# Performance work log

Measured on AMD Instinct MI355X. Metric: run time of the kernel, lower is better.

Reference implementation:

```python
import jax, jax.numpy as jnp
import numpy as np
from jax import lax

B, T = 32, 768
N_MEL = 80
ENC_POS = 544  # encoder_output_dim(512) + positional_embedding_dim(32)
PRE = 256
RNN = 1024


def setup_inputs() -> dict:
    key = jax.random.key(0)
    ks = jax.random.split(key, 12)
    n = lambda k, shape, s: jax.random.normal(k, shape, jnp.float32) * s
    return {
        'duration_outputs': n(ks[0], (B, T, ENC_POS), 1.0),
        'decoder_inputs': n(ks[1], (B, N_MEL, T), 1.0),
        'memory_lengths': jax.random.randint(ks[2], (B,), 1, T + 1, dtype=jnp.int32),
        'pre_w1': n(ks[3], (N_MEL, PRE), 0.05),
        'pre_w2': n(ks[4], (PRE, PRE), 0.05),
        'rnn1_wx': n(ks[5], (PRE + ENC_POS, 4 * RNN), 0.02),
        'rnn1_wh': n(ks[6], (RNN, 4 * RNN), 0.02),
        'rnn1_b': jnp.zeros(4 * RNN, jnp.float32),
        'rnn1_g': jnp.ones(4 * RNN, jnp.float32),
        'rnn1_bn': jnp.zeros(4 * RNN, jnp.float32),
        'rnn1_gc': jnp.ones(RNN, jnp.float32),
        'rnn1_bc': jnp.zeros(RNN, jnp.float32),
        'rnn2_wx': n(ks[7], (RNN, 4 * RNN), 0.02),
        'rnn2_wh': n(ks[8], (RNN, 4 * RNN), 0.02),
        'rnn2_b': jnp.zeros(4 * RNN, jnp.float32),
        'rnn2_g': jnp.ones(4 * RNN, jnp.float32),
        'rnn2_bn': jnp.zeros(4 * RNN, jnp.float32),
        'rnn2_gc': jnp.ones(RNN, jnp.float32),
        'rnn2_bc': jnp.zeros(RNN, jnp.float32),
        'proj_w': n(ks[9], (RNN + ENC_POS, N_MEL), 0.02),
        'proj_b': jnp.zeros(N_MEL, jnp.float32),
    }


def _ln(x, g, b):
    m = jnp.mean(x, axis=-1, keepdims=True)
    v = jnp.var(x, axis=-1, keepdims=True)
    return (x - m) * lax.rsqrt(v + 1e-5) * g + b


def _lstm_norm_cell(x, h, c, wx, wh, b, g, bn, gc, bc):
    # layer-normalized LSTM cell: LN over gate pre-activations + LN on cell
    z = _ln(x @ wx + h @ wh + b, g, bn)            # [B, 4H]
    i, f, gg, o = jnp.split(z, 4, axis=-1)
    c = jax.nn.sigmoid(f) * c + jax.nn.sigmoid(i) * jnp.tanh(gg)
    h = jax.nn.sigmoid(o) * jnp.tanh(_ln(c, gc, bc))
    return h, c


def reference(duration_outputs, decoder_inputs, memory_lengths,
              pre_w1, pre_w2,
              rnn1_wx, rnn1_wh, rnn1_b, rnn1_g, rnn1_bn, rnn1_gc, rnn1_bc,
              rnn2_wx, rnn2_wh, rnn2_b, rnn2_g, rnn2_bn, rnn2_gc, rnn2_bc,
              proj_w, proj_b):
    b = decoder_inputs.shape[0]
    t = decoder_inputs.shape[2]
    # parse_decoder_inputs: [B, M, T] -> [T, B, M]; prepend go frame
    dec = jnp.transpose(decoder_inputs, (2, 0, 1))
    dec = jnp.concatenate([jnp.zeros((1, b, N_MEL), dec.dtype), dec], axis=0)  # [T+1,B,M]
    # prenet (dropout disabled for deterministic reference)
    x = jax.nn.relu(dec @ pre_w1)
    x = jax.nn.relu(x @ pre_w2)
    pre = x[:t]                                            # [T, B, PRE]
    dur = jnp.transpose(duration_outputs, (1, 0, 2))       # [T, B, ENC_POS]

    def step(carry, xs):
        h1, c1, h2, c2 = carry
        p, d = xs
        cell_in = jnp.concatenate([p, d], axis=-1)
        h1, c1 = _lstm_norm_cell(cell_in, h1, c1, rnn1_wx, rnn1_wh, rnn1_b, rnn1_g, rnn1_bn, rnn1_gc, rnn1_bc)
        h2, c2 = _lstm_norm_cell(h1, h2, c2, rnn2_wx, rnn2_wh, rnn2_b, rnn2_g, rnn2_bn, rnn2_gc, rnn2_bc)
        out = jnp.concatenate([h2, d], axis=-1) @ proj_w + proj_b  # [B, M]
        return (h1, c1, h2, c2), out

    init = tuple(jnp.zeros((b, RNN), jnp.float32) for _ in range(4))
    _, mel = lax.scan(step, init, (pre, dur))              # [T, B, M]
    return jnp.transpose(mel, (1, 2, 0))                   # [B, M, T]
```

## Files before the change

### kernel.cpp

```cpp
#include <hip/hip_runtime.h>
#include <cstdint>
#include <cstddef>

typedef _Float16 f16;
typedef _Float16 f16x8 __attribute__((ext_vector_type(8)));
typedef float f32x4 __attribute__((ext_vector_type(4)));

#define MFMA_F16(a,b,c) __builtin_amdgcn_mfma_f32_16x16x32_f16((a),(b),(c),0,0,0)

#define LOG2E  1.4426950408889634f
#define LOG2E2 2.885390081777927f

__device__ __forceinline__ float sigf(float x){
  return __builtin_amdgcn_rcpf(1.f + exp2f(-x * LOG2E));
}
__device__ __forceinline__ float tanhfast(float x){
  float e = exp2f(x * LOG2E2);
  return fmaf(-2.f, __builtin_amdgcn_rcpf(e + 1.f), 1.f);
}

__device__ __forceinline__ void st_wt_f32(float* p, float v){
  asm volatile("global_store_dword %0, %1, off sc0 sc1" :: "v"(p), "v"(v) : "memory");
}
__device__ __forceinline__ void st_wt_u32(f16* p, unsigned v){
  asm volatile("global_store_dword %0, %1, off sc0 sc1" :: "v"(p), "v"(v) : "memory");
}
__device__ __forceinline__ void st_tag(unsigned* p, unsigned v){
  asm volatile("global_store_dword %0, %1, off sc0 sc1" :: "v"(p), "v"(v) : "memory");
}
__device__ __forceinline__ void tag_wait(const unsigned* p, unsigned target){
  for (;;){
    unsigned v;
    asm volatile("global_load_dword %0, %1, off sc0 sc1\n\ts_waitcnt vmcnt(0)"
                 : "=v"(v) : "v"(p) : "memory");
    if (v >= target) return;
    __builtin_amdgcn_s_sleep(1);
  }
}
__device__ __forceinline__ void vm_drain(){ asm volatile("s_waitcnt vmcnt(0)" ::: "memory"); }

template<int N> __device__ __forceinline__ void vm_waitN(){
  asm volatile("s_waitcnt vmcnt(%0)" :: "i"(N) : "memory");
  __builtin_amdgcn_sched_barrier(0);
}

__device__ __forceinline__ void ld_8f32(const float* p, f32x4& a, f32x4& b){
  asm volatile(
    "global_load_dwordx4 %0, %2, off sc0 sc1\n\t"
    "global_load_dwordx4 %1, %2, off offset:16 sc0 sc1\n\t"
    "s_waitcnt vmcnt(0)"
    : "=&v"(a), "=&v"(b) : "v"(p) : "memory");
}

__device__ __forceinline__ void ld8_issue(const f16* p, f16x8* f){
  asm volatile(
    "global_load_dwordx4 %0, %8, off sc0 sc1\n\t"
    "global_load_dwordx4 %1, %8, off offset:64 sc0 sc1\n\t"
    "global_load_dwordx4 %2, %8, off offset:128 sc0 sc1\n\t"
    "global_load_dwordx4 %3, %8, off offset:192 sc0 sc1\n\t"
    "global_load_dwordx4 %4, %8, off offset:256 sc0 sc1\n\t"
    "global_load_dwordx4 %5, %8, off offset:320 sc0 sc1\n\t"
    "global_load_dwordx4 %6, %8, off offset:384 sc0 sc1\n\t"
    "global_load_dwordx4 %7, %8, off offset:448 sc0 sc1"
    : "=&v"(f[0]),"=&v"(f[1]),"=&v"(f[2]),"=&v"(f[3]),
      "=&v"(f[4]),"=&v"(f[5]),"=&v"(f[6]),"=&v"(f[7])
    : "v"(p) : "memory");
}

__device__ __forceinline__ f32x4 gemm32r(const f16* hp, const f16x8* bfrag){
  f32x4 a = {0.f,0.f,0.f,0.f};
  f16x8 fA[8], fB[8];
  ld8_issue(hp,       fA);
  ld8_issue(hp + 256, fB);
  vm_waitN<8>();
  #pragma unroll
  for (int kk = 0; kk < 8; ++kk) a = MFMA_F16(fA[kk], bfrag[kk], a);
  ld8_issue(hp + 512, fA);
  vm_waitN<8>();
  #pragma unroll
  for (int kk = 0; kk < 8; ++kk) a = MFMA_F16(fB[kk], bfrag[8 + kk], a);
  ld8_issue(hp + 768, fB);
  vm_waitN<8>();
  #pragma unroll
  for (int kk = 0; kk < 8; ++kk) a = MFMA_F16(fA[kk], bfrag[16 + kk], a);
  vm_waitN<0>();
  #pragma unroll
  for (int kk = 0; kk < 8; ++kk) a = MFMA_F16(fB[kk], bfrag[24 + kk], a);
  return a;
}

__global__ __launch_bounds__(256) void k_transpose_f16(const float* __restrict__ src,
    f16* __restrict__ dst, int K, int N, int dstStride, int dstOff){
  const int n0 = blockIdx.x*32, k0 = blockIdx.y*32, tid = threadIdx.x;
  __shared__ float tl[32][33];
  #pragma unroll
  for (int rep = 0; rep < 4; ++rep){
    int e = rep*256 + tid; int i = e >> 5, j = e & 31;
    int k = k0 + i, n = n0 + j;
    tl[i][j] = (k < K && n < N) ? src[(size_t)k*N + n] : 0.f;
  }
  __syncthreads();
  #pragma unroll
  for (int rep = 0; rep < 4; ++rep){
    int e = rep*256 + tid; int i2 = e & 31, j2 = e >> 5;
    int n = n0 + j2, k = k0 + i2;
    if (k < K && n < N) dst[(size_t)n*dstStride + dstOff + k] = (f16)tl[i2][j2];
  }
}

__global__ __launch_bounds__(256) void k_prenet(const float* __restrict__ dec,
    const float* __restrict__ w1, const float* __restrict__ w2, f16* __restrict__ cellin){
  const int t = blockIdx.x, tid = threadIdx.x;
  __shared__ float sin_[32][81];
  __shared__ f16   w1T[256][88];
  __shared__ float x1s[32][260];
  __shared__ f16   w2c[256][72];
  __shared__ f16   xo[32][256];
  for (int e = tid; e < 32*80; e += 256){
    int i = e/80, m = e - i*80;
    sin_[i][m] = (t == 0) ? 0.f : dec[(size_t)i*61440 + (size_t)m*768 + (t-1)];
  }
  for (int e = tid; e < 80*256; e += 256){ int m = e >> 8, j = e & 255; w1T[j][m] = (f16)w1[e]; }
  __syncthreads();
  const int j = tid;
  for (int i = 0; i < 32; ++i){
    float a = 0.f;
    #pragma unroll
    for (int m8 = 0; m8 < 10; ++m8){
      f16x8 wvv = *(const f16x8*)&w1T[j][m8*8];
      #pragma unroll
      for (int l = 0; l < 8; ++l) a += (float)wvv[l] * sin_[i][m8*8 + l];
    }
    x1s[i][j] = fmaxf(a, 0.f);
  }
  __syncthreads();
  float acc2[32];
  #pragma unroll
  for (int i = 0; i < 32; ++i) acc2[i] = 0.f;
  for (int c = 0; c < 4; ++c){
    for (int e = tid; e < 64*256; e += 256){
      int kl = e >> 8, jj = e & 255;
      w2c[jj][kl] = (f16)w2[(size_t)(c*64 + kl)*256 + jj];
    }
    __syncthreads();
    f16x8 wv8[8];
    #pragma unroll
    for (int k8 = 0; k8 < 8; ++k8) wv8[k8] = *(const f16x8*)&w2c[j][k8*8];
    for (int i = 0; i < 32; ++i){
      float a = 0.f;
      #pragma unroll
      for (int k8 = 0; k8 < 8; ++k8)
        #pragma unroll
        for (int l = 0; l < 8; ++l) a += (float)wv8[k8][l]*x1s[i][c*64 + k8*8 + l];
      acc2[i] += a;
    }
    __syncthreads();
  }
  for (int i = 0; i < 32; ++i) xo[i][j] = (f16)fmaxf(acc2[i], 0.f);
  __syncthreads();
  for (int e = tid; e < 32*256; e += 256){
    int i = e >> 8, jj = e & 255;
    cellin[((size_t)t*32 + i)*800 + jj] = xo[i][jj];
  }
}

__global__ __launch_bounds__(256) void k_durfill(const float* __restrict__ dur, f16* __restrict__ cellin){
  const int t = blockIdx.x, tid = threadIdx.x;
  for (int e = tid; e < 32*544; e += 256){
    int b = e / 544, c = e - b*544;
    cellin[((size_t)t*32 + b)*800 + 256 + c] = (f16)dur[(size_t)b*417792 + (size_t)t*544 + c];
  }
}

__global__ __launch_bounds__(256) void k_ws_report(float* __restrict__ out, int n, float val){
  int i = blockIdx.x*256 + threadIdx.x;
  if (i < n) out[i] = val;
}

__global__ __launch_bounds__(512, 1) void k_recurrence(
    const f16* __restrict__ cellin, const f16* __restrict__ wxT1,
    const f16* __restrict__ whT1, const f16* __restrict__ w2T,
    f16* __restrict__ H2all, f16* __restrict__ h1buf, f16* __restrict__ h2buf,
    float* __restrict__ zbuf1, float* __restrict__ zbuf2,
    unsigned* __restrict__ tags,
    const float* __restrict__ b1v,
    const float* __restrict__ g1, const float* __restrict__ bn1,
    const float* __restrict__ gc1v, const float* __restrict__ bc1v,
    const float* __restrict__ b2v,
    const float* __restrict__ g2, const float* __restrict__ bn2,
    const float* __restrict__ gc2v, const float* __restrict__ bc2v)
{
  const int tid = threadIdx.x, blk = blockIdx.x;
  const int lane = tid & 63, wv = tid >> 6;
  const int r16 = lane & 15, quad = lane >> 4;
  const int part = wv >> 2, pair = wv & 3, rt = pair >> 1, ct = pair & 1;
  const int g_b = ct*2 + (r16 >> 3), u_b = r16 & 7;
  const int zrow = tid >> 4, zc0 = tid & 15, zc1 = (tid & 15) + 16;
  const int zrt = zrow >> 4, zi = zrow & 15;
  const int arow = rt*16 + r16;

  unsigned* ztag1 = tags;
  unsigned* ztag2 = tags + 2048;
  unsigned* htag1 = tags + 4096;
  unsigned* htag2 = tags + 4608;
  unsigned* ctag  = tags + 5120;

  __shared__ f16   swx[3200*8];
  __shared__ float zredA[8][16][17];
  __shared__ float zredX[2][4][16][17];
  __shared__ float zs[4096];
  __shared__ float wredS1[8], wredQ1[8], wredS2[8], wredQ2[8];

  f16x8 bfrag[32];

  if (blk < 128){
    const int ub0 = blk*8;
    const int colg = (g_b << 10) + ub0 + u_b;
    if (part == 0){
      #pragma unroll
      for (int c = 0; c < 32; ++c)
        bfrag[c] = *(const f16x8*)(whT1 + (size_t)colg*1024 + c*32 + quad*8);
    }
    for (int idx = tid; idx < 3200; idx += 512){
      int l = idx & 15, q = (idx >> 4) & 3, v = idx >> 6;
      int c = v % 25, ctx = v / 25;
      int gg = ctx*2 + (l >> 3), uu = l & 7;
      int cg = (gg << 10) + ub0 + uu;
      *(f16x8*)(swx + idx*8) = *(const f16x8*)(wxT1 + (size_t)cg*800 + c*32 + q*8);
    }
    const float zb0 = b1v[((zc0 >> 3) << 10) + ub0 + (zc0 & 7)];
    const float zb1 = b1v[((zc1 >> 3) << 10) + ub0 + (zc1 & 7)];
    float pgv[4][2], pbv[4][2], gcv[2], bcv[2], cst[2] = {0.f, 0.f};
    if (blk < 32){
      #pragma unroll
      for (int k = 0; k < 2; ++k){
        const int u = 2*tid + k;
        #pragma unroll
        for (int g = 0; g < 4; ++g){
          pgv[g][k] = g1[(g << 10) + u]; pbv[g][k] = bn1[(g << 10) + u];
        }
        gcv[k] = gc1v[u]; bcv[k] = bc1v[u];
      }
    }
    __syncthreads();
    if (part == 1){
      f32x4 a = {0.f,0.f,0.f,0.f};
      const f16* ap = cellin + (size_t)arow*800 + quad*8;
      for (int c = 0; c < 25; ++c){
        f16x8 av = *(const f16x8*)(ap + c*32);
        f16x8 bx = *(const f16x8*)(swx + (size_t)(((ct*25 + c)*4 + quad)*16 + r16)*8);
        a = MFMA_F16(av, bx, a);
      }
      #pragma unroll
      for (int reg = 0; reg < 4; ++reg) zredX[0][wv-4][quad*4 + reg][r16] = a[reg];
    }
    for (int t = 0; t < 768; ++t){
      if (part == 0){
        if (t > 0){
          tag_wait(htag1 + arow*16, (unsigned)t);
          const f16* hp = h1buf + (size_t)((t-1)&3)*32768 + (size_t)arow*1024 + quad*8;
          f32x4 a = gemm32r(hp, bfrag);
          #pragma unroll
          for (int reg = 0; reg < 4; ++reg) zredA[wv][quad*4 + reg][r16] = a[reg];
        } else {
          #pragma unroll
          for (int reg = 0; reg < 4; ++reg) zredA[wv][quad*4 + reg][r16] = 0.f;
        }
      } else if (t < 767){
        f32x4 a = {0.f,0.f,0.f,0.f};
        const f16* ap = cellin + (size_t)(t+1)*25600 + (size_t)arow*800 + quad*8;
        for (int c = 0; c < 25; ++c){
          f16x8 av = *(const f16x8*)(ap + c*32);
          f16x8 bx = *(const f16x8*)(swx + (size_t)(((ct*25 + c)*4 + quad)*16 + r16)*8);
          a = MFMA_F16(av, bx, a);
        }
        #pragma unroll
        for (int reg = 0; reg < 4; ++reg) zredX[(t+1)&1][wv-4][quad*4 + reg][r16] = a[reg];
      }
      __syncthreads();
      {
        const int xs = t & 1;
        float za  = zredA[zrt*2    ][zi][zc0] + zredX[xs][zrt*2    ][zi][zc0] + zb0;
        float zbv = zredA[zrt*2 + 1][zi][zc0] + zredX[xs][zrt*2 + 1][zi][zc0] + zb1;
        float* zp = zbuf1 + (size_t)zrow*4096;
        st_wt_f32(zp + ((zc0 >> 3) << 10) + ub0 + (zc0 & 7), za);
        st_wt_f32(zp + ((zc1 >> 3) << 10) + ub0 + (zc1 & 7), zbv);
      }
      vm_drain(); __syncthreads();
      if (tid == 0) st_tag(ztag1 + blk*16, (unsigned)(t+1));
      if (blk < 32){
        if (t >= 4 && tid >= 256 && tid < 384)
          tag_wait(ctag + (tid-256)*16, (unsigned)(t-3));
        tag_wait(ztag1 + (tid & 127)*16, (unsigned)(t+1));
        f32x4 va, vb;
        ld_8f32(zbuf1 + (size_t)blk*4096 + tid*8, va, vb);
        *(f32x4*)(zs + tid*8)     = va;
        *(f32x4*)(zs + tid*8 + 4) = vb;
        float s = va.x+va.y+va.z+va.w + vb.x+vb.y+vb.z+vb.w;
        float q = va.x*va.x+va.y*va.y+va.z*va.z+va.w*va.w
                + vb.x*vb.x+vb.y*vb.y+vb.z*vb.z+vb.w*vb.w;
        s += __shfl_down(s, 32); q += __shfl_down(q, 32);
        s += __shfl_down(s, 16); q += __shfl_down(q, 16);
        s += __shfl_down(s, 8);  q += __shfl_down(q, 8);
        s += __shfl_down(s, 4);  q += __shfl_down(q, 4);
        s += __shfl_down(s, 2);  q += __shfl_down(q, 2);
        s += __shfl_down(s, 1);  q += __shfl_down(q, 1);
        if (lane == 0){ wredS1[wv] = s; wredQ1[wv] = q; }
        __syncthreads();
        float S = 0.f, Q = 0.f;
        #pragma unroll
        for (int w = 0; w < 8; ++w){ S += wredS1[w]; Q += wredQ1[w]; }
        const float m1 = S * (1.f/4096.f);
        const float rs1 = rsqrtf(Q*(1.f/4096.f) - m1*m1 + 1e-5f);
        float oo[2];
        #pragma unroll
        for (int k = 0; k < 2; ++k){
          const int u = 2*tid + k;
          const float ziv = (zs[u]        - m1)*rs1*pgv[0][k] + pbv[0][k];
          const float zf  = (zs[1024 + u] - m1)*rs1*pgv[1][k] + pbv[1][k];
          const float zg  = (zs[2048 + u] - m1)*rs1*pgv[2][k] + pbv[2][k];
          const float zo  = (zs[3072 + u] - m1)*rs1*pgv[3][k] + pbv[3][k];
          cst[k] = sigf(zf)*cst[k] + sigf(ziv)*tanhfast(zg);
          oo[k] = sigf(zo);
        }
        float s2 = cst[0] + cst[1], q2 = cst[0]*cst[0] + cst[1]*cst[1];
        s2 += __shfl_down(s2, 32); q2 += __shfl_down(q2, 32);
        s2 += __shfl_down(s2, 16); q2 += __shfl_down(q2, 16);
        s2 += __shfl_down(s2, 8);  q2 += __shfl_down(q2, 8);
        s2 += __shfl_down(s2, 4);  q2 += __shfl_down(q2, 4);
        s2 += __shfl_down(s2, 2);  q2 += __shfl_down(q2, 2);
        s2 += __shfl_down(s2, 1);  q2 += __shfl_down(q2, 1);
        if (lane == 0){ wredS2[wv] = s2; wredQ2[wv] = q2; }
        __syncthreads();
        float S2 = 0.f, Q2 = 0.f;
        #pragma unroll
        for (int w = 0; w < 8; ++w){ S2 += wredS2[w]; Q2 += wredQ2[w]; }
        const float m2 = S2 * (1.f/1024.f);
        const float rs2 = rsqrtf(Q2*(1.f/1024.f) - m2*m2 + 1e-5f);
        union { f16 f[2]; unsigned u32v; } pk;
        #pragma unroll
        for (int k = 0; k < 2; ++k){
          float arg = fmaf(fmaf(cst[k], rs2, -m2*rs2), gcv[k], bcv[k]);
          float e = exp2f(arg * LOG2E2);
          pk.f[k] = (f16)(oo[k] * fmaf(-2.f, __builtin_amdgcn_rcpf(e + 1.f), 1.f));
        }
        st_wt_u32(h1buf + (size_t)(t&3)*32768 + blk*1024 + 2*tid, pk.u32v);
        vm_drain(); __syncthreads();
        if (tid == 0) st_tag(htag1 + blk*16, (unsigned)(t+1));
      }
    }
  } else {
    const int blk2 = blk - 128, ub0 = blk2*8;
    const int colg = (g_b << 10) + ub0 + u_b;
    {
      const f16* wsrc = w2T + (size_t)colg*2048 + (part == 0 ? 1024 : 0);
      #pragma unroll
      for (int c = 0; c < 32; ++c)
        bfrag[c] = *(const f16x8*)(wsrc + c*32 + quad*8);
    }
    const float zb0 = b2v[((zc0 >> 3) << 10) + ub0 + (zc0 & 7)];
    const float zb1 = b2v[((zc1 >> 3) << 10) + ub0 + (zc1 & 7)];
    float pgv[4][2], pbv[4][2], gcv[2], bcv[2], cst[2] = {0.f, 0.f};
    if (blk2 < 32){
      #pragma unroll
      for (int k = 0; k < 2; ++k){
        const int u = 2*tid + k;
        #pragma unroll
        for (int g = 0; g < 4; ++g){
          pgv[g][k] = g2[(g << 10) + u]; pbv[g][k] = bn2[(g << 10) + u];
        }
        gcv[k] = gc2v[u]; bcv[k] = bc2v[u];
      }
    }
    __syncthreads();
    for (int t = 0; t < 768; ++t){
      if (part == 0){
        if (t > 0){
          tag_wait(htag2 + arow*16, (unsigned)t);
          const f16* hp = h2buf + (size_t)((t+1)&1)*32768 + (size_t)arow*1024 + quad*8;
          f32x4 a = gemm32r(hp, bfrag);
          #pragma unroll
          for (int reg = 0; reg < 4; ++reg) zredA[wv][quad*4 + reg][r16] = a[reg];
        } else {
          #pragma unroll
          for (int reg = 0; reg < 4; ++reg) zredA[wv][quad*4 + reg][r16] = 0.f;
        }
      } else {
        tag_wait(htag1 + arow*16, (unsigned)(t+1));
        const f16* hp = h1buf + (size_t)(t&3)*32768 + (size_t)arow*1024 + quad*8;
        f32x4 a = gemm32r(hp, bfrag);
        #pragma unroll
        for (int reg = 0; reg < 4; ++reg) zredA[wv][quad*4 + reg][r16] = a[reg];
      }
      __syncthreads();
      if (tid == 0) st_tag(ctag + blk2*16, (unsigned)(t+1));
      {
        float za  = zredA[zrt*2    ][zi][zc0] + zredA[4 + zrt*2    ][zi][zc0] + zb0;
        float zbv = zredA[zrt*2 + 1][zi][zc0] + zredA[4 + zrt*2 + 1][zi][zc0] + zb1;
        float* zp = zbuf2 + (size_t)zrow*4096;
        st_wt_f32(zp + ((zc0 >> 3) << 10) + ub0 + (zc0 & 7), za);
        st_wt_f32(zp + ((zc1 >> 3) << 10) + ub0 + (zc1 & 7), zbv);
      }
      vm_drain(); __syncthreads();
      if (tid == 0) st_tag(ztag2 + blk2*16, (unsigned)(t+1));
      if (blk2 < 32){
        tag_wait(ztag2 + (tid & 127)*16, (unsigned)(t+1));
        f32x4 va, vb;
        ld_8f32(zbuf2 + (size_t)blk2*4096 + tid*8, va, vb);
        *(f32x4*)(zs + tid*8)     = va;
        *(f32x4*)(zs + tid*8 + 4) = vb;
        float s = va.x+va.y+va.z+va.w + vb.x+vb.y+vb.z+vb.w;
        float q = va.x*va.x+va.y*va.y+va.z*va.z+va.w*va.w
                + vb.x*vb.x+vb.y*vb.y+vb.z*vb.z+vb.w*vb.w;
        s += __shfl_down(s, 32); q += __shfl_down(q, 32);
        s += __shfl_down(s, 16); q += __shfl_down(q, 16);
        s += __shfl_down(s, 8);  q += __shfl_down(q, 8);
        s += __shfl_down(s, 4);  q += __shfl_down(q, 4);
        s += __shfl_down(s, 2);  q += __shfl_down(q, 2);
        s += __shfl_down(s, 1);  q += __shfl_down(q, 1);
        if (lane == 0){ wredS1[wv] = s; wredQ1[wv] = q; }
        __syncthreads();
        float S = 0.f, Q = 0.f;
        #pragma unroll
        for (int w = 0; w < 8; ++w){ S += wredS1[w]; Q += wredQ1[w]; }
        const float m1 = S * (1.f/4096.f);
        const float rs1 = rsqrtf(Q*(1.f/4096.f) - m1*m1 + 1e-5f);
        float oo[2];
        #pragma unroll
        for (int k = 0; k < 2; ++k){
          const int u = 2*tid + k;
          const float ziv = (zs[u]        - m1)*rs1*pgv[0][k] + pbv[0][k];
          const float zf  = (zs[1024 + u] - m1)*rs1*pgv[1][k] + pbv[1][k];
          const float zg  = (zs[2048 + u] - m1)*rs1*pgv[2][k] + pbv[2][k];
          const float zo  = (zs[3072 + u] - m1)*rs1*pgv[3][k] + pbv[3][k];
          cst[k] = sigf(zf)*cst[k] + sigf(ziv)*tanhfast(zg);
          oo[k] = sigf(zo);
        }
        float s2 = cst[0] + cst[1], q2 = cst[0]*cst[0] + cst[1]*cst[1];
        s2 += __shfl_down(s2, 32); q2 += __shfl_down(q2, 32);
        s2 += __shfl_down(s2, 16); q2 += __shfl_down(q2, 16);
        s2 += __shfl_down(s2, 8);  q2 += __shfl_down(q2, 8);
        s2 += __shfl_down(s2, 4);  q2 += __shfl_down(q2, 4);
        s2 += __shfl_down(s2, 2);  q2 += __shfl_down(q2, 2);
        s2 += __shfl_down(s2, 1);  q2 += __shfl_down(q2, 1);
        if (lane == 0){ wredS2[wv] = s2; wredQ2[wv] = q2; }
        __syncthreads();
        float S2 = 0.f, Q2 = 0.f;
        #pragma unroll
        for (int w = 0; w < 8; ++w){ S2 += wredS2[w]; Q2 += wredQ2[w]; }
        const float m2 = S2 * (1.f/1024.f);
        const float rs2 = rsqrtf(Q2*(1.f/1024.f) - m2*m2 + 1e-5f);
        union { f16 f[2]; unsigned u32v; } pk;
        #pragma unroll
        for (int k = 0; k < 2; ++k){
          float arg = fmaf(fmaf(cst[k], rs2, -m2*rs2), gcv[k], bcv[k]);
          float e = exp2f(arg * LOG2E2);
          pk.f[k] = (f16)(oo[k] * fmaf(-2.f, __builtin_amdgcn_rcpf(e + 1.f), 1.f));
        }
        st_wt_u32(h2buf + (size_t)(t&1)*32768 + blk2*1024 + 2*tid, pk.u32v);
        st_wt_u32(H2all + (size_t)(t+1)*32768 + blk2*1024 + 2*tid, pk.u32v);
        vm_drain(); __syncthreads();
        if (tid == 0) st_tag(htag2 + blk2*16, (unsigned)(t+1));
      }
    }
  }
}

__global__ __launch_bounds__(256) void k_proj(const f16* __restrict__ H2all, const f16* __restrict__ cellin,
    const f16* __restrict__ projT, const float* __restrict__ projb, float* __restrict__ out){
  const int t = blockIdx.x, tid = threadIdx.x;
  const int lane = tid & 63, wv = tid >> 6;
  const int r16 = lane & 15, quad = lane >> 4;
  __shared__ float pred[4][32][84];
  f32x4 acc[2][5] = {};
  const f16* H2 = H2all + (size_t)(t+1)*32768;
  const f16* CI = cellin + (size_t)t*32*800;
  const int kbeg = wv*13;
  const int kend = (wv == 3) ? 49 : (kbeg + 13);
  for (int ks = kbeg; ks < kend; ++ks){
    const int k0 = ks*32 + quad*8;
    f16x8 a0, a1;
    if (ks < 32){
      a0 = *(const f16x8*)(H2 + r16*1024 + k0);
      a1 = *(const f16x8*)(H2 + (16+r16)*1024 + k0);
    } else {
      a0 = *(const f16x8*)(CI + r16*800 + 256 + (k0 - 1024));
      a1 = *(const f16x8*)(CI + (16+r16)*800 + 256 + (k0 - 1024));
    }
    f16x8 bf[5];
    #pragma unroll
    for (int nt = 0; nt < 5; ++nt)
      bf[nt] = *(const f16x8*)(projT + (size_t)(nt*16 + r16)*1568 + k0);
    #pragma unroll
    for (int nt = 0; nt < 5; ++nt){
      acc[0][nt] = MFMA_F16(a0, bf[nt], acc[0][nt]);
      acc[1][nt] = MFMA_F16(a1, bf[nt], acc[1][nt]);
    }
  }
  #pragma unroll
  for (int mt = 0; mt < 2; ++mt)
    #pragma unroll
    for (int nt = 0; nt < 5; ++nt)
      #pragma unroll
      for (int reg = 0; reg < 4; ++reg)
        pred[wv][mt*16 + quad*4 + reg][nt*16 + r16] = acc[mt][nt][reg];
  __syncthreads();
  for (int e = tid; e < 2560; e += 256){
    int m = e >> 5, b = e & 31;
    float v = pred[0][b][m] + pred[1][b][m] + pred[2][b][m] + pred[3][b][m] + projb[m];
    out[(size_t)b*61440 + (size_t)m*768 + t] = v;
  }
}

extern "C" void kernel_launch(void* const* d_in, const int* in_sizes, int n_in,
                              void* d_out, int out_size, void* d_ws, size_t ws_size,
                              hipStream_t stream)
{
  const float* duration = (const float*)d_in[0];
  const float* decoder  = (const float*)d_in[1];
  const float* pre_w1   = (const float*)d_in[3];
  const float* pre_w2   = (const float*)d_in[4];
  const float* rnn1_wx  = (const float*)d_in[5];
  const float* rnn1_wh  = (const float*)d_in[6];
  const float* rnn1_b   = (const float*)d_in[7];
  const float* rnn1_g   = (const float*)d_in[8];
  const float* rnn1_bn  = (const float*)d_in[9];
  const float* rnn1_gc  = (const float*)d_in[10];
  const float* rnn1_bc  = (const float*)d_in[11];
  const float* rnn2_wx  = (const float*)d_in[12];
  const float* rnn2_wh  = (const float*)d_in[13];
  const float* rnn2_b   = (const float*)d_in[14];
  const float* rnn2_g   = (const float*)d_in[15];
  const float* rnn2_bn  = (const float*)d_in[16];
  const float* rnn2_gc  = (const float*)d_in[17];
  const float* rnn2_bc  = (const float*)d_in[18];
  const float* proj_w   = (const float*)d_in[19];
  const float* proj_b   = (const float*)d_in[20];
  float* out = (float*)d_out;

  char* w = (char*)d_ws;
  f16* cellin = (f16*)w;      w += (size_t)24576*800*2;
  f16* wxT1   = (f16*)w;      w += (size_t)4096*800*2;
  f16* whT1   = (f16*)w;      w += (size_t)4096*1024*2;
  f16* w2T    = (f16*)w;      w += (size_t)4096*2048*2;
  f16* projT  = (f16*)w;      w += 262144;
  f16* H2all  = (f16*)w;      w += (size_t)769*32768*2;
  f16* h1buf  = (f16*)w;      w += 262144;
  f16* h2buf  = (f16*)w;      w += 131072;
  float* zbuf1 = (float*)w;   w += (size_t)32*4096*4;
  float* zbuf2 = (float*)w;   w += (size_t)32*4096*4;
  unsigned* tags = (unsigned*)w; w += 28672;
  const size_t need = (size_t)((char*)w - (char*)d_ws);
  if (ws_size < need){
    k_ws_report<<<(out_size + 255)/256, 256, 0, stream>>>(out, out_size, (float)(ws_size >> 20));
    return;
  }

  (void)hipMemsetAsync(tags, 0, 28672, stream);
  (void)hipMemsetAsync(h1buf, 0, 262144, stream);
  (void)hipMemsetAsync(h2buf, 0, 131072, stream);

  k_transpose_f16<<<dim3(4096/32, 25), 256, 0, stream>>>(rnn1_wx, wxT1, 800, 4096, 800, 0);
  k_transpose_f16<<<dim3(4096/32, 32), 256, 0, stream>>>(rnn1_wh, whT1, 1024, 4096, 1024, 0);
  k_transpose_f16<<<dim3(4096/32, 32), 256, 0, stream>>>(rnn2_wx, w2T, 1024, 4096, 2048, 0);
  k_transpose_f16<<<dim3(4096/32, 32), 256, 0, stream>>>(rnn2_wh, w2T, 1024, 4096, 2048, 1024);
  k_transpose_f16<<<dim3(3, 49), 256, 0, stream>>>(proj_w, projT, 1568, 80, 1568, 0);
  k_prenet<<<768, 256, 0, stream>>>(decoder, pre_w1, pre_w2, cellin);
  k_durfill<<<768, 256, 0, stream>>>(duration, cellin);
  k_recurrence<<<256, 512, 0, stream>>>(cellin, wxT1, whT1, w2T, H2all, h1buf, h2buf,
      zbuf1, zbuf2, tags,
      rnn1_b, rnn1_g, rnn1_bn, rnn1_gc, rnn1_bc,
      rnn2_b, rnn2_g, rnn2_bn, rnn2_gc, rnn2_bc);
  k_proj<<<768, 256, 0, stream>>>(H2all, cellin, projT, proj_b, out);
}
```

Baseline: 9.706 ms.

## Split recurrent K dimension across both wave groups in LSTM persistent blocks

Work in both layers is now split along the reduction dimension instead of by role. Previously one group of waves did the full 1024-long recurrent h@Wh GEMM while the other did the input projection. Now each half of the waves handles 512 of K for the h-GEMM, and in layer 1 also half of the x-projection, with partial results summed through shared memory. In layer 1 the next step's x-projection moves after the h-update, taking it off the critical path before the tag signal. The aim is to halve latency on the serial recurrent path, at the cost of extra shared-memory reductions and more register pressure from holding two 16-fragment weight sets in layer 2.

```diff
diff --git a/kernel.cpp b/kernel.cpp
--- a/kernel.cpp
+++ b/kernel.cpp
@@ -67,7 +67,7 @@
     : "v"(p) : "memory");
 }
 
-__device__ __forceinline__ f32x4 gemm32r(const f16* hp, const f16x8* bfrag){
+__device__ __forceinline__ f32x4 gemm16(const f16* hp, const f16x8* bfrag){
   f32x4 a = {0.f,0.f,0.f,0.f};
   f16x8 fA[8], fB[8];
   ld8_issue(hp,       fA);
@@ -75,17 +75,9 @@
   vm_waitN<8>();
   #pragma unroll
   for (int kk = 0; kk < 8; ++kk) a = MFMA_F16(fA[kk], bfrag[kk], a);
-  ld8_issue(hp + 512, fA);
-  vm_waitN<8>();
+  vm_waitN<0>();
   #pragma unroll
   for (int kk = 0; kk < 8; ++kk) a = MFMA_F16(fB[kk], bfrag[8 + kk], a);
-  ld8_issue(hp + 768, fB);
-  vm_waitN<8>();
-  #pragma unroll
-  for (int kk = 0; kk < 8; ++kk) a = MFMA_F16(fA[kk], bfrag[16 + kk], a);
-  vm_waitN<0>();
-  #pragma unroll
-  for (int kk = 0; kk < 8; ++kk) a = MFMA_F16(fB[kk], bfrag[24 + kk], a);
   return a;
 }
 
@@ -207,20 +199,17 @@
 
   __shared__ f16   swx[3200*8];
   __shared__ float zredA[8][16][17];
-  __shared__ float zredX[2][4][16][17];
+  __shared__ float zredX[2][8][16][17];
   __shared__ float zs[4096];
   __shared__ float wredS1[8], wredQ1[8], wredS2[8], wredQ2[8];
-
-  f16x8 bfrag[32];
 
   if (blk < 128){
     const int ub0 = blk*8;
     const int colg = (g_b << 10) + ub0 + u_b;
-    if (part == 0){
-      #pragma unroll
-      for (int c = 0; c < 32; ++c)
-        bfrag[c] = *(const f16x8*)(whT1 + (size_t)colg*1024 + c*32 + quad*8);
-    }
+    f16x8 bfrag[16];
+    #pragma unroll
+    for (int c2 = 0; c2 < 16; ++c2)
+      bfrag[c2] = *(const f16x8*)(whT1 + (size_t)colg*1024 + (part*16 + c2)*32 + quad*8);
     for (int idx = tid; idx < 3200; idx += 512){
       int l = idx & 15, q = (idx >> 4) & 3, v = idx >> 6;
       int c = v % 25, ctx = v / 25;
@@ -230,6 +219,7 @@
     }
     const float zb0 = b1v[((zc0 >> 3) << 10) + ub0 + (zc0 & 7)];
     const float zb1 = b1v[((zc1 >> 3) << 10) + ub0 + (zc1 & 7)];
+    const int cbeg = part ? 12 : 0, cend = part ? 25 : 12;
     float pgv[4][2], pbv[4][2], gcv[2], bcv[2], cst[2] = {0.f, 0.f};
     if (blk < 32){
       #pragma unroll
@@ -243,45 +233,35 @@
       }
     }
     __syncthreads();
-    if (part == 1){
+    {
       f32x4 a = {0.f,0.f,0.f,0.f};
       const f16* ap = cellin + (size_t)arow*800 + quad*8;
-      for (int c = 0; c < 25; ++c){
+      for (int c = cbeg; c < cend; ++c){
         f16x8 av = *(const f16x8*)(ap + c*32);
         f16x8 bx = *(const f16x8*)(swx + (size_t)(((ct*25 + c)*4 + quad)*16 + r16)*8);
         a = MFMA_F16(av, bx, a);
       }
       #pragma unroll
-      for (int reg = 0; reg < 4; ++reg) zredX[0][wv-4][quad*4 + reg][r16] = a[reg];
+      for (int reg = 0; reg < 4; ++reg) zredX[0][wv][quad*4 + reg][r16] = a[reg];
     }
     for (int t = 0; t < 768; ++t){
-      if (part == 0){
-        if (t > 0){
-          tag_wait(htag1 + arow*16, (unsigned)t);
-          const f16* hp = h1buf + (size_t)((t-1)&3)*32768 + (size_t)arow*1024 + quad*8;
-          f32x4 a = gemm32r(hp, bfrag);
-          #pragma unroll
-          for (int reg = 0; reg < 4; ++reg) zredA[wv][quad*4 + reg][r16] = a[reg];
-        } else {
-          #pragma unroll
-          for (int reg = 0; reg < 4; ++reg) zredA[wv][quad*4 + reg][r16] = 0.f;
-        }
-      } else if (t < 767){
-        f32x4 a = {0.f,0.f,0.f,0.f};
-        const f16* ap = cellin + (size_t)(t+1)*25600 + (size_t)arow*800 + quad*8;
-        for (int c = 0; c < 25; ++c){
-          f16x8 av = *(const f16x8*)(ap + c*32);
-          f16x8 bx = *(const f16x8*)(swx + (size_t)(((ct*25 + c)*4 + quad)*16 + r16)*8);
-          a = MFMA_F16(av, bx, a);
-        }
-        #pragma unroll
-        for (int reg = 0; reg < 4; ++reg) zredX[(t+1)&1][wv-4][quad*4 + reg][r16] = a[reg];
+      if (t > 0){
+        tag_wait(htag1 + arow*16, (unsigned)t);
+        const f16* hp = h1buf + (size_t)((t-1)&3)*32768 + (size_t)arow*1024 + part*512 + quad*8;
+        f32x4 a = gemm16(hp, bfrag);
+        #pragma unroll
+        for (int reg = 0; reg < 4; ++reg) zredA[wv][quad*4 + reg][r16] = a[reg];
+      } else {
+        #pragma unroll
+        for (int reg = 0; reg < 4; ++reg) zredA[wv][quad*4 + reg][r16] = 0.f;
       }
       __syncthreads();
       {
         const int xs = t & 1;
-        float za  = zredA[zrt*2    ][zi][zc0] + zredX[xs][zrt*2    ][zi][zc0] + zb0;
-        float zbv = zredA[zrt*2 + 1][zi][zc0] + zredX[xs][zrt*2 + 1][zi][zc0] + zb1;
+        float za  = zredA[zrt*2    ][zi][zc0] + zredA[4 + zrt*2    ][zi][zc0]
+                  + zredX[xs][zrt*2    ][zi][zc0] + zredX[xs][4 + zrt*2    ][zi][zc0] + zb0;
+        float zbv = zredA[zrt*2 + 1][zi][zc0] + zredA[4 + zrt*2 + 1][zi][zc0]
+                  + zredX[xs][zrt*2 + 1][zi][zc0] + zredX[xs][4 + zrt*2 + 1][zi][zc0] + zb1;
         float* zp = zbuf1 + (size_t)zrow*4096;
         st_wt_f32(zp + ((zc0 >> 3) << 10) + ub0 + (zc0 & 7), za);
         st_wt_f32(zp + ((zc1 >> 3) << 10) + ub0 + (zc1 & 7), zbv);
@@ -348,15 +328,26 @@
         vm_drain(); __syncthreads();
         if (tid == 0) st_tag(htag1 + blk*16, (unsigned)(t+1));
       }
+      if (t < 767){
+        f32x4 a = {0.f,0.f,0.f,0.f};
+        const f16* ap = cellin + (size_t)(t+1)*25600 + (size_t)arow*800 + quad*8;
+        for (int c = cbeg; c < cend; ++c){
+          f16x8 av = *(const f16x8*)(ap + c*32);
+          f16x8 bx = *(const f16x8*)(swx + (size_t)(((ct*25 + c)*4 + quad)*16 + r16)*8);
+          a = MFMA_F16(av, bx, a);
+        }
+        #pragma unroll
+        for (int reg = 0; reg < 4; ++reg) zredX[(t+1)&1][wv][quad*4 + reg][r16] = a[reg];
+      }
     }
   } else {
     const int blk2 = blk - 128, ub0 = blk2*8;
     const int colg = (g_b << 10) + ub0 + u_b;
-    {
-      const f16* wsrc = w2T + (size_t)colg*2048 + (part == 0 ? 1024 : 0);
-      #pragma unroll
-      for (int c = 0; c < 32; ++c)
-        bfrag[c] = *(const f16x8*)(wsrc + c*32 + quad*8);
+    f16x8 bfragH[16], bfragX[16];
+    #pragma unroll
+    for (int c2 = 0; c2 < 16; ++c2){
+      bfragH[c2] = *(const f16x8*)(w2T + (size_t)colg*2048 + 1024 + (part*16 + c2)*32 + quad*8);
+      bfragX[c2] = *(const f16x8*)(w2T + (size_t)colg*2048 +        (part*16 + c2)*32 + quad*8);
     }
     const float zb0 = b2v[((zc0 >> 3) << 10) + ub0 + (zc0 & 7)];
     const float zb1 = b2v[((zc1 >> 3) << 10) + ub0 + (zc1 & 7)];
@@ -374,29 +365,30 @@
     }
     __syncthreads();
     for (int t = 0; t < 768; ++t){
-      if (part == 0){
-        if (t > 0){
-          tag_wait(htag2 + arow*16, (unsigned)t);
-          const f16* hp = h2buf + (size_t)((t+1)&1)*32768 + (size_t)arow*1024 + quad*8;
-          f32x4 a = gemm32r(hp, bfrag);
-          #pragma unroll
-          for (int reg = 0; reg < 4; ++reg) zredA[wv][quad*4 + reg][r16] = a[reg];
-        } else {
-          #pragma unroll
-          for (int reg = 0; reg < 4; ++reg) zredA[wv][quad*4 + reg][r16] = 0.f;
-        }
+      if (t > 0){
+        tag_wait(htag2 + arow*16, (unsigned)t);
+        const f16* hp = h2buf + (size_t)((t+1)&1)*32768 + (size_t)arow*1024 + part*512 + quad*8;
+        f32x4 a = gemm16(hp, bfragH);
+        #pragma unroll
+        for (int reg = 0; reg < 4; ++reg) zredX[0][wv][quad*4 + reg][r16] = a[reg];
       } else {
+        #pragma unroll
+        for (int reg = 0; reg < 4; ++reg) zredX[0][wv][quad*4 + reg][r16] = 0.f;
+      }
+      {
         tag_wait(htag1 + arow*16, (unsigned)(t+1));
-        const f16* hp = h1buf + (size_t)(t&3)*32768 + (size_t)arow*1024 + quad*8;
-        f32x4 a = gemm32r(hp, bfrag);
+        const f16* hp = h1buf + (size_t)(t&3)*32768 + (size_t)arow*1024 + part*512 + quad*8;
+        f32x4 a = gemm16(hp, bfragX);
         #pragma unroll
         for (int reg = 0; reg < 4; ++reg) zredA[wv][quad*4 + reg][r16] = a[reg];
       }
       __syncthreads();
       if (tid == 0) st_tag(ctag + blk2*16, (unsigned)(t+1));
       {
-        float za  = zredA[zrt*2    ][zi][zc0] + zredA[4 + zrt*2    ][zi][zc0] + zb0;
-        float zbv = zredA[zrt*2 + 1][zi][zc0] + zredA[4 + zrt*2 + 1][zi][zc0] + zb1;
+        float za  = zredA[zrt*2    ][zi][zc0] + zredA[4 + zrt*2    ][zi][zc0]
+                  + zredX[0][zrt*2    ][zi][zc0] + zredX[0][4 + zrt*2    ][zi][zc0] + zb0;
+        float zbv = zredA[zrt*2 + 1][zi][zc0] + zredA[4 + zrt*2 + 1][zi][zc0]
+                  + zredX[0][zrt*2 + 1][zi][zc0] + zredX[0][4 + zrt*2 + 1][zi][zc0] + zb1;
         float* zp = zbuf2 + (size_t)zrow*4096;
         st_wt_f32(zp + ((zc0 >> 3) << 10) + ub0 + (zc0 & 7), za);
         st_wt_f32(zp + ((zc1 >> 3) << 10) + ub0 + (zc1 & 7), zbv);
```

Result: slower. 10.51 ms (+8.3%).
